# Performance work log

Hardware: AMD Instinct MI355X
Metric: run time of the kernel (lower is better)

## Reference

```python
import jax, jax.numpy as jnp
import numpy as np
from jax import lax

EPS = 1e-5

def binarize(x):
    # sign() forward, straight-through (identity) backward, like BinarizeConv2d's .data trick
    return x + lax.stop_gradient(jnp.sign(x) - x)

def conv_nchw(x, w, stride, pad):
    return lax.conv_general_dilated(
        x, w, window_strides=(stride, stride), padding=((pad, pad), (pad, pad)),
        dimension_numbers=('NCHW', 'OIHW', 'NCHW'))

def batchnorm_train(x, gamma, beta):
    # training-mode BN: per-channel batch mean / biased variance over (N,H,W)
    mean = jnp.mean(x, axis=(0, 2, 3), keepdims=True)
    var = jnp.mean((x - mean) ** 2, axis=(0, 2, 3), keepdims=True)
    xhat = (x - mean) * lax.rsqrt(var + EPS)
    return xhat * gamma[None, :, None, None] + beta[None, :, None, None]

def hardtanh(x):
    return jnp.clip(x, -1.0, 1.0)

def setup_inputs() -> dict:
    key = jax.random.key(0)
    ks = jax.random.split(key, 7)
    N, Cin, Cout, H, W = 32, 64, 64, 128, 128
    x = jax.random.normal(ks[0], (N, Cin, H, W), dtype=jnp.float32)
    w1 = jax.random.normal(ks[1], (Cout, Cin, 3, 3), dtype=jnp.float32) * 0.05
    w2 = jax.random.normal(ks[2], (Cout, Cout, 3, 3), dtype=jnp.float32) * 0.05
    g1 = jnp.ones((Cout,), dtype=jnp.float32)
    b1 = jnp.zeros((Cout,), dtype=jnp.float32)
    g2 = jnp.ones((Cout,), dtype=jnp.float32)
    b2 = jnp.zeros((Cout,), dtype=jnp.float32)
    return {"x": x, "w1": w1, "g1": g1, "b1": b1, "w2": w2, "g2": g2, "b2": b2}

def reference(x, w1, g1, b1, w2, g2, b2):
    # conv1: binarized input (C=64 != 3) and binarized weights
    out = conv_nchw(binarize(x), binarize(w1), stride=1, pad=1)
    out = hardtanh(batchnorm_train(out, g1, b1))
    # conv2: 3x3, stride 1 (stride==1 branch)
    out = conv_nchw(binarize(out), binarize(w2), stride=1, pad=1)
    out = batchnorm_train(out, g2, b2)
    # identity shortcut (stride==1 and in_planes==planes)
    out = out + x
    return hardtanh(out)
```

## Files before the change

### kernel.cpp

```cpp
#include <hip/hip_runtime.h>
#include <stdint.h>

typedef unsigned long long u64;
typedef unsigned int u32;

#define Nn 32
#define Cc 64
#define Hh 128
#define Ww 128
#define HPAD 130
#define WPAD 130
#define NHW_TOT (Nn*Hh*Ww)
#define NBIN 16

__device__ __forceinline__ float2 compute_ab(const u64* __restrict__ sum, const u64* __restrict__ sq,
        const float* __restrict__ g, const float* __restrict__ bet, int c) {
    long long Sv = 0, Qv = 0;
    #pragma unroll
    for (int b = 0; b < NBIN; ++b) {
        Sv += (long long)sum[b * 64 + c];
        Qv += (long long)sq[b * 64 + c];
    }
    double mean = (double)Sv / (double)NHW_TOT;
    double var = (double)Qv / (double)NHW_TOT - mean * mean;
    double invstd = 1.0 / sqrt(var + 1e-5);
    double a = (double)g[c] * invstd;
    double b_ = (double)bet[c] - a * mean;
    return make_float2((float)a, (float)b_);
}

#define BORDER_PER_IMG 516
#define BORDER_TOT (Nn * BORDER_PER_IMG)
#define PREP_EXTRA (1152 + 2 * BORDER_TOT + 4 * NBIN * 64)

__global__ __launch_bounds__(256) void prep_kernel(const float* __restrict__ x,
        const float* __restrict__ w1, const float* __restrict__ w2,
        u64* __restrict__ xpad, u64* __restrict__ ypad,
        u64* __restrict__ w1b, u64* __restrict__ w2b, u64* __restrict__ stats) {
    if (blockIdx.x < 512) {
        int t = blockIdx.x * 256 + threadIdx.x;
        int P = t * 4;
        int row = P >> 7, w0 = P & 127;
        int n = row >> 7, h = row & 127;
        const float4* xp4 = (const float4*)(x + ((size_t)n * Cc * Hh + h) * Ww + w0);
        u32 lo0 = 0, lo1 = 0, lo2 = 0, lo3 = 0, hi0 = 0, hi1 = 0, hi2 = 0, hi3 = 0;
        #pragma unroll 8
        for (int c = 0; c < 32; ++c) {
            float4 v = xp4[c * (Hh * Ww / 4)];
            lo0 |= (__float_as_uint(v.x) >> 31) << c;
            lo1 |= (__float_as_uint(v.y) >> 31) << c;
            lo2 |= (__float_as_uint(v.z) >> 31) << c;
            lo3 |= (__float_as_uint(v.w) >> 31) << c;
        }
        #pragma unroll 8
        for (int c = 32; c < 64; ++c) {
            float4 v = xp4[c * (Hh * Ww / 4)];
            hi0 |= (__float_as_uint(v.x) >> 31) << (c - 32);
            hi1 |= (__float_as_uint(v.y) >> 31) << (c - 32);
            hi2 |= (__float_as_uint(v.z) >> 31) << (c - 32);
            hi3 |= (__float_as_uint(v.w) >> 31) << (c - 32);
        }
        u64* dst = xpad + ((size_t)n * HPAD + h + 1) * WPAD + w0 + 1;
        dst[0] = ((u64)hi0 << 32) | lo0;
        dst[1] = ((u64)hi1 << 32) | lo1;
        dst[2] = ((u64)hi2 << 32) | lo2;
        dst[3] = ((u64)hi3 << 32) | lo3;
    } else {
        int t = (blockIdx.x - 512) * 256 + threadIdx.x;
        int stride = (gridDim.x - 512) * 256;
        for (int i = t; i < PREP_EXTRA; i += stride) {
            if (i < 1152) {
                int set = i / 576, idx = i - set * 576;
                const float* src = set ? w2 : w1;
                u64* db = set ? w2b : w1b;
                int co = idx / 9, tap = idx - co * 9;
                const float* p = src + (size_t)co * 576 + tap;
                u32 lo = 0, hi = 0;
                #pragma unroll
                for (int ci = 0; ci < 32; ++ci)
                    lo |= (__float_as_uint(p[ci * 9]) >> 31) << ci;
                #pragma unroll
                for (int ci = 32; ci < 64; ++ci)
                    hi |= (__float_as_uint(p[ci * 9]) >> 31) << (ci - 32);
                db[idx] = ((u64)hi << 32) | lo;
            } else if (i < 1152 + 2 * BORDER_TOT) {
                int z = i - 1152;
                u64* buf = (z < BORDER_TOT) ? xpad : ypad;
                int k = (z < BORDER_TOT) ? z : z - BORDER_TOT;
                int img = k / BORDER_PER_IMG, j = k - img * BORDER_PER_IMG;
                size_t base = (size_t)img * HPAD * WPAD;
                size_t off;
                if (j < 130)      off = j;
                else if (j < 260) off = (size_t)(HPAD - 1) * WPAD + (j - 130);
                else {
                    int k2 = j - 260;
                    off = (size_t)(1 + (k2 >> 1)) * WPAD + ((k2 & 1) ? (WPAD - 1) : 0);
                }
                buf[base + off] = 0ull;
            } else {
                stats[i - 1152 - 2 * BORDER_TOT] = 0ull;
            }
        }
    }
}

__device__ __forceinline__ void conv4(const u64* __restrict__ L0, const u64* __restrict__ L1,
                                      const u64* __restrict__ L2, int w,
                                      const u64 W[9], int corrMid, int v[4]) {
    u64 a[6], b[6], c[6];
    #pragma unroll
    for (int j = 0; j < 6; ++j) { a[j] = L0[w + j]; b[j] = L1[w + j]; c[j] = L2[w + j]; }
    #pragma unroll
    for (int px = 0; px < 4; ++px) {
        int p0 = __popcll(a[px] ^ W[0]) + __popcll(a[px + 1] ^ W[1]) + __popcll(a[px + 2] ^ W[2]);
        int p1 = __popcll(b[px] ^ W[3]) + __popcll(b[px + 1] ^ W[4]) + __popcll(b[px + 2] ^ W[5]);
        int p2 = __popcll(c[px] ^ W[6]) + __popcll(c[px + 1] ^ W[7]) + __popcll(c[px + 2] ^ W[8]);
        v[px] = 576 - 2 * (p0 + p1 + p2) - corrMid;
    }
}

struct LaneCtx {
    u64 W[9];
    int corrMid, corrW0, corrW127;
};

__device__ __forceinline__ void lane_setup(LaneCtx& C, const u64* __restrict__ wb,
                                           int lane, int h) {
    #pragma unroll
    for (int t = 0; t < 9; ++t) C.W[t] = wb[lane * 9 + t];
    int wc[9];
    #pragma unroll
    for (int t = 0; t < 9; ++t) wc[t] = 64 - 2 * __popcll(C.W[t]);
    int tT = wc[0] + wc[1] + wc[2], tB = wc[6] + wc[7] + wc[8];
    int tL = wc[0] + wc[3] + wc[6], tR = wc[2] + wc[5] + wc[8];
    bool fT = (h == 0), fB = (h == 127);
    C.corrMid  = (fT ? tT : 0) + (fB ? tB : 0);
    C.corrW0   = tL - (fT ? wc[0] : 0) - (fB ? wc[6] : 0);
    C.corrW127 = tR - (fT ? wc[2] : 0) - (fB ? wc[8] : 0);
}

__device__ __forceinline__ void load_win(u64* __restrict__ win, const u64* __restrict__ inpad,
                                         int n, int hp, int half, int tid) {
    const u64* src = inpad + ((size_t)n * HPAD + hp * 2) * WPAD + half * 64;
    for (int i = tid; i < 264; i += 128) {
        int r = i / 66, c = i - r * 66;
        win[r * 68 + c] = src[(size_t)r * WPAD + c];
    }
}

__global__ __launch_bounds__(128) void conv_stats(const u64* __restrict__ inpad,
        const u64* __restrict__ wb, u64* __restrict__ gsum, u64* __restrict__ gsq) {
    __shared__ u64 win[4 * 68];
    __shared__ int r32[256];
    int tid = threadIdx.x;
    int lane = tid & 63;
    int wv = __builtin_amdgcn_readfirstlane(tid >> 6);
    int blk = blockIdx.x;
    int half = blk & 1;
    int hp = (blk >> 1) & 63;
    int n = blk >> 7;
    int h = hp * 2 + wv;
    load_win(win, inpad, n, hp, half, tid);
    LaneCtx C;
    lane_setup(C, wb, lane, h);
    __syncthreads();
    const u64* L0 = &win[wv * 68];
    const u64* L1 = L0 + 68;
    const u64* L2 = L0 + 136;
    int s = 0, q = 0;
    for (int w = 0; w < 64; w += 4) {
        int v[4];
        conv4(L0, L1, L2, w, C.W, C.corrMid, v);
        if (half == 0 && w == 0)  v[0] -= C.corrW0;
        if (half == 1 && w == 60) v[3] -= C.corrW127;
        #pragma unroll
        for (int px = 0; px < 4; ++px) {
            s += v[px];
            q += __mul24(v[px], v[px]);
        }
    }
    __syncthreads();
    r32[wv * 64 + lane] = s;
    r32[128 + wv * 64 + lane] = q;
    __syncthreads();
    if (wv == 0) {
        int S = r32[lane] + r32[64 + lane];
        int Q = r32[128 + lane] + r32[192 + lane];
        int bin = blk & (NBIN - 1);
        atomicAdd(&gsum[bin * 64 + lane], (u64)(long long)S);
        atomicAdd(&gsq[bin * 64 + lane], (u64)(long long)Q);
    }
}

__global__ __launch_bounds__(128) void signpack_h(const u64* __restrict__ inpad,
        const u64* __restrict__ wb, const u64* __restrict__ sum, const u64* __restrict__ sq,
        const float* __restrict__ g, const float* __restrict__ bet,
        u64* __restrict__ ypad) {
    __shared__ u64 win[4 * 68];
    int tid = threadIdx.x;
    int lane = tid & 63;
    int wv = __builtin_amdgcn_readfirstlane(tid >> 6);
    int blk = blockIdx.x;
    int half = blk & 1;
    int hp = (blk >> 1) & 63;
    int n = blk >> 7;
    int h = hp * 2 + wv;
    load_win(win, inpad, n, hp, half, tid);
    LaneCtx C;
    lane_setup(C, wb, lane, h);
    float2 ab = compute_ab(sum, sq, g, bet, lane);
    __syncthreads();
    const u64* L0 = &win[wv * 68];
    const u64* L1 = L0 + 68;
    const u64* L2 = L0 + 136;
    u64 myw = 0;
    for (int w = 0; w < 64; w += 4) {
        int v[4];
        conv4(L0, L1, L2, w, C.W, C.corrMid, v);
        if (half == 0 && w == 0)  v[0] -= C.corrW0;
        if (half == 1 && w == 60) v[3] -= C.corrW127;
        #pragma unroll
        for (int px = 0; px < 4; ++px) {
            float t = fmaf((float)v[px], ab.x, ab.y);
            u64 bal = __ballot(t < 0.0f);
            if (lane == w + px) myw = bal;
        }
    }
    ypad[((size_t)n * HPAD + h + 1) * WPAD + 1 + half * 64 + lane] = myw;
}

__global__ __launch_bounds__(128) void final5_kernel(const u64* __restrict__ inpad,
        const u64* __restrict__ wb, const u64* __restrict__ sum, const u64* __restrict__ sq,
        const float* __restrict__ g, const float* __restrict__ bet,
        const float* __restrict__ x, float* __restrict__ out) {
    __shared__ u64 win[4 * 68];
    __shared__ short T[2][64 * 36];
    __shared__ float2 absh[64];
    int tid = threadIdx.x;
    int lane = tid & 63;
    int wv = __builtin_amdgcn_readfirstlane(tid >> 6);
    int blk = blockIdx.x;
    int half = blk & 1;
    int hp = (blk >> 1) & 63;
    int n = blk >> 7;
    int h = hp * 2 + wv;
    load_win(win, inpad, n, hp, half, tid);
    LaneCtx C;
    lane_setup(C, wb, lane, h);
    if (tid < 64) absh[tid] = compute_ab(sum, sq, g, bet, tid);
    __syncthreads();
    const u64* L0 = &win[wv * 68];
    const u64* L1 = L0 + 68;
    const u64* L2 = L0 + 136;
    short* Tw = T[wv];
    int p4 = lane & 7;
    int cosub = lane >> 3;
    size_t base_nch = ((size_t)n * Cc * Hh + h) * Ww;
    for (int w = 0; w < 64; w += 4) {
        int v[4];
        conv4(L0, L1, L2, w, C.W, C.corrMid, v);
        if (half == 0 && w == 0)  v[0] -= C.corrW0;
        if (half == 1 && w == 60) v[3] -= C.corrW127;
        short4 sv;
        sv.x = (short)v[0]; sv.y = (short)v[1]; sv.z = (short)v[2]; sv.w = (short)v[3];
        *(short4*)&Tw[lane * 36 + (w & 31)] = sv;
        if ((w & 31) == 28) {
            int w0g = half * 64 + (w & ~31);
            #pragma unroll 8
            for (int st = 0; st < 8; ++st) {
                int co = st * 8 + cosub;
                short4 tv = *(const short4*)&Tw[co * 36 + p4 * 4];
                float2 cab = absh[co];
                size_t idx = base_nch + (size_t)co * (Hh * Ww) + w0g + p4 * 4;
                float4 xv = *(const float4*)(x + idx);
                float4 yv;
                yv.x = fminf(1.0f, fmaxf(-1.0f, fmaf((float)tv.x, cab.x, cab.y) + xv.x));
                yv.y = fminf(1.0f, fmaxf(-1.0f, fmaf((float)tv.y, cab.x, cab.y) + xv.y));
                yv.z = fminf(1.0f, fmaxf(-1.0f, fmaf((float)tv.z, cab.x, cab.y) + xv.z));
                yv.w = fminf(1.0f, fmaxf(-1.0f, fmaf((float)tv.w, cab.x, cab.y) + xv.w));
                *(float4*)(out + idx) = yv;
            }
        }
    }
}

extern "C" void kernel_launch(void* const* d_in, const int* in_sizes, int n_in,
                              void* d_out, int out_size, void* d_ws, size_t ws_size,
                              hipStream_t stream) {
    const float* x  = (const float*)d_in[0];
    const float* w1 = (const float*)d_in[1];
    const float* g1 = (const float*)d_in[2];
    const float* b1 = (const float*)d_in[3];
    const float* w2 = (const float*)d_in[4];
    const float* g2 = (const float*)d_in[5];
    const float* b2 = (const float*)d_in[6];
    float* out = (float*)d_out;
    char* ws = (char*)d_ws;

    constexpr size_t SZ_PAD   = (size_t)Nn * HPAD * WPAD * sizeof(u64);
    constexpr size_t OFF_YPAD = SZ_PAD;
    constexpr size_t OFF_STAT = 2 * SZ_PAD;
    constexpr size_t SZ_STAT  = (size_t)NBIN * 64 * 8;
    constexpr size_t OFF_W1B  = OFF_STAT + 4 * SZ_STAT;
    constexpr size_t OFF_W2B  = OFF_W1B + 576 * 8;
    constexpr size_t WS_NEEDED = OFF_W2B + 576 * 8;

    if (ws_size < WS_NEEDED) return;

    u64* xpad = (u64*)(ws);
    u64* ypad = (u64*)(ws + OFF_YPAD);
    u64* stats = (u64*)(ws + OFF_STAT);
    u64* gsum1 = (u64*)(ws + OFF_STAT);
    u64* gsq1  = (u64*)(ws + OFF_STAT + SZ_STAT);
    u64* gsum2 = (u64*)(ws + OFF_STAT + 2 * SZ_STAT);
    u64* gsq2  = (u64*)(ws + OFF_STAT + 3 * SZ_STAT);
    u64* w1b  = (u64*)(ws + OFF_W1B);
    u64* w2b  = (u64*)(ws + OFF_W2B);

    prep_kernel<<<530, 256, 0, stream>>>(x, w1, w2, xpad, ypad, w1b, w2b, stats);
    conv_stats<<<4096, 128, 0, stream>>>(xpad, w1b, gsum1, gsq1);
    signpack_h<<<4096, 128, 0, stream>>>(xpad, w1b, gsum1, gsq1, g1, b1, ypad);
    conv_stats<<<4096, 128, 0, stream>>>(ypad, w2b, gsum2, gsq2);
    final5_kernel<<<4096, 128, 0, stream>>>(ypad, w2b, gsum2, gsq2, g2, b2, x, out);
}
```

Measured before the change: 234.0 us.

## Spill conv1 results to int16 buffer instead of recomputing for sign packing

When enough workspace is available, the first conv+stats kernel stores each pre-BN conv output as int16. A new signpack_v kernel then applies BN and sign-packs from that buffer rather than recomputing the binary convolution. This trades the popcount recompute for a large extra write and read of global memory. Shared-memory window loads in conv4 are also widened to 16-byte vector loads.

```diff
diff --git a/kernel.cpp b/kernel.cpp
--- a/kernel.cpp
+++ b/kernel.cpp
@@ -109,7 +109,14 @@
                                       const u64 W[9], int corrMid, int v[4]) {
     u64 a[6], b[6], c[6];
     #pragma unroll
-    for (int j = 0; j < 6; ++j) { a[j] = L0[w + j]; b[j] = L1[w + j]; c[j] = L2[w + j]; }
+    for (int j = 0; j < 3; ++j) {
+        ulonglong2 pa = *(const ulonglong2*)&L0[w + 2 * j];
+        ulonglong2 pb = *(const ulonglong2*)&L1[w + 2 * j];
+        ulonglong2 pc = *(const ulonglong2*)&L2[w + 2 * j];
+        a[2 * j] = pa.x; a[2 * j + 1] = pa.y;
+        b[2 * j] = pb.x; b[2 * j + 1] = pb.y;
+        c[2 * j] = pc.x; c[2 * j + 1] = pc.y;
+    }
     #pragma unroll
     for (int px = 0; px < 4; ++px) {
         int p0 = __popcll(a[px] ^ W[0]) + __popcll(a[px + 1] ^ W[1]) + __popcll(a[px + 2] ^ W[2]);
@@ -148,8 +155,10 @@
     }
 }
 
-__global__ __launch_bounds__(128) void conv_stats(const u64* __restrict__ inpad,
-        const u64* __restrict__ wb, u64* __restrict__ gsum, u64* __restrict__ gsq) {
+template<bool SPILL>
+__global__ __launch_bounds__(128) void conv_statsT(const u64* __restrict__ inpad,
+        const u64* __restrict__ wb, u64* __restrict__ gsum, u64* __restrict__ gsq,
+        short* __restrict__ v16) {
     __shared__ u64 win[4 * 68];
     __shared__ int r32[256];
     int tid = threadIdx.x;
@@ -167,6 +176,7 @@
     const u64* L0 = &win[wv * 68];
     const u64* L1 = L0 + 68;
     const u64* L2 = L0 + 136;
+    short* vrow = SPILL ? (v16 + (((size_t)(n * Hh + h) * Ww) + half * 64) * 64 + lane) : nullptr;
     int s = 0, q = 0;
     for (int w = 0; w < 64; w += 4) {
         int v[4];
@@ -177,6 +187,7 @@
         for (int px = 0; px < 4; ++px) {
             s += v[px];
             q += __mul24(v[px], v[px]);
+            if (SPILL) vrow[(size_t)(w + px) * 64] = (short)v[px];
         }
     }
     __syncthreads();
@@ -190,6 +201,29 @@
         atomicAdd(&gsum[bin * 64 + lane], (u64)(long long)S);
         atomicAdd(&gsq[bin * 64 + lane], (u64)(long long)Q);
     }
+}
+
+__global__ __launch_bounds__(256) void signpack_v(const short* __restrict__ v16,
+        const u64* __restrict__ sum, const u64* __restrict__ sq,
+        const float* __restrict__ g, const float* __restrict__ bet,
+        u64* __restrict__ ypad) {
+    int tid = threadIdx.x;
+    int lane = tid & 63;
+    int wv = tid >> 6;
+    int grow = blockIdx.x * 2 + (wv >> 1);
+    int base = (wv & 1) * 64;
+    int n = grow >> 7, h = grow & 127;
+    float2 ab = compute_ab(sum, sq, g, bet, lane);
+    const short* vr = v16 + ((size_t)grow * Ww + base) * 64;
+    u64* drow = ypad + ((size_t)n * HPAD + h + 1) * WPAD + 1;
+    u64 myw = 0;
+    #pragma unroll 8
+    for (int px = 0; px < 64; ++px) {
+        float tv = fmaf((float)vr[(size_t)px * 64 + lane], ab.x, ab.y);
+        u64 bal = __ballot(tv < 0.0f);
+        if (lane == px) myw = bal;
+    }
+    drow[base + lane] = myw;
 }
 
 __global__ __launch_bounds__(128) void signpack_h(const u64* __restrict__ inpad,
@@ -303,9 +337,13 @@
     constexpr size_t SZ_STAT  = (size_t)NBIN * 64 * 8;
     constexpr size_t OFF_W1B  = OFF_STAT + 4 * SZ_STAT;
     constexpr size_t OFF_W2B  = OFF_W1B + 576 * 8;
-    constexpr size_t WS_NEEDED = OFF_W2B + 576 * 8;
-
-    if (ws_size < WS_NEEDED) return;
+    constexpr size_t OFF_V16  = OFF_W2B + 576 * 8;
+    constexpr size_t SZ_V16   = (size_t)Nn * Hh * Ww * 64 * 2;
+    constexpr size_t WS_SMALL = OFF_V16;
+    constexpr size_t WS_FULL  = OFF_V16 + SZ_V16;
+
+    if (ws_size < WS_SMALL) return;
+    bool spill = (ws_size >= WS_FULL);
 
     u64* xpad = (u64*)(ws);
     u64* ypad = (u64*)(ws + OFF_YPAD);
@@ -316,10 +354,16 @@
     u64* gsq2  = (u64*)(ws + OFF_STAT + 3 * SZ_STAT);
     u64* w1b  = (u64*)(ws + OFF_W1B);
     u64* w2b  = (u64*)(ws + OFF_W2B);
+    short* v16 = (short*)(ws + OFF_V16);
 
     prep_kernel<<<530, 256, 0, stream>>>(x, w1, w2, xpad, ypad, w1b, w2b, stats);
-    conv_stats<<<4096, 128, 0, stream>>>(xpad, w1b, gsum1, gsq1);
-    signpack_h<<<4096, 128, 0, stream>>>(xpad, w1b, gsum1, gsq1, g1, b1, ypad);
-    conv_stats<<<4096, 128, 0, stream>>>(ypad, w2b, gsum2, gsq2);
+    if (spill) {
+        conv_statsT<true><<<4096, 128, 0, stream>>>(xpad, w1b, gsum1, gsq1, v16);
+        signpack_v<<<2048, 256, 0, stream>>>(v16, gsum1, gsq1, g1, b1, ypad);
+    } else {
+        conv_statsT<false><<<4096, 128, 0, stream>>>(xpad, w1b, gsum1, gsq1, nullptr);
+        signpack_h<<<4096, 128, 0, stream>>>(xpad, w1b, gsum1, gsq1, g1, b1, ypad);
+    }
+    conv_statsT<false><<<4096, 128, 0, stream>>>(ypad, w2b, gsum2, gsq2, nullptr);
     final5_kernel<<<4096, 128, 0, stream>>>(ypad, w2b, gsum2, gsq2, g2, b2, x, out);
 }
```

Measured after the change: 209.4 us. 1.12x faster.
